# Kernel optimization log

Measured on AMD Instinct MI355X. Metric: run time of the kernel, lower is better.

Reference implementation:

```python
import jax, jax.numpy as jnp
import numpy as np

B, N, D, S = 16, 128, 128, 128   # batch, n_nodes, node/edge feat dim, state_dim
MP_INT = 256
UP_INT = 256
EPS = 1e-3  # keras BatchNormalization default epsilon


def _mlp(x, W1, b1, W2, b2):
    # Dense(relu) -> Dense(relu)
    h = jax.nn.relu(x @ W1 + b1)
    return jax.nn.relu(h @ W2 + b2)


def setup_inputs() -> dict:
    key = jax.random.key(0)
    ks = jax.random.split(key, 16)
    g = lambda k, shape: jax.random.normal(k, shape, dtype=jnp.float32) * 0.05
    nodes = jax.random.normal(ks[0], (B, N, D), dtype=jnp.float32)
    edges = jax.random.normal(ks[1], (B, N * N, D), dtype=jnp.float32)
    mask = (jax.random.uniform(ks[2], (B, N * N, 1)) > 0.5).astype(jnp.float32)
    return {
        "nodes": nodes, "edges": edges, "mask": mask,
        # Adj_Updater_1: concat(node_i, node_j, edge_ij) -> UP_INT -> S
        "W1a": g(ks[3], (3 * D, UP_INT)), "b1a": jnp.zeros((UP_INT,), jnp.float32),
        "W2a": g(ks[4], (UP_INT, S)), "b2a": jnp.zeros((S,), jnp.float32),
        # Message_Passer_1: concat(node_i, node_j, new_edge) -> MP_INT -> S
        "W1m": g(ks[5], (2 * D + S, MP_INT)), "b1m": jnp.zeros((MP_INT,), jnp.float32),
        "W2m": g(ks[6], (MP_INT, S)), "b2m": jnp.zeros((S,), jnp.float32),
        # Update_Func_1: concat(old_state, agg_messages) -> UP_INT -> S
        "W1u": g(ks[7], (D + S, UP_INT)), "b1u": jnp.zeros((UP_INT,), jnp.float32),
        "W2u": g(ks[8], (UP_INT, S)), "b2u": jnp.zeros((S,), jnp.float32),
        # BatchNorm (inference mode: moving stats) for nodes and edges
        "gamma_n": jnp.ones((S,), jnp.float32), "beta_n": jnp.zeros((S,), jnp.float32),
        "mean_n": jnp.zeros((S,), jnp.float32), "var_n": jnp.ones((S,), jnp.float32),
        "gamma_e": jnp.ones((S,), jnp.float32), "beta_e": jnp.zeros((S,), jnp.float32),
        "mean_e": jnp.zeros((S,), jnp.float32), "var_e": jnp.ones((S,), jnp.float32),
    }


def reference(nodes, edges, mask,
              W1a, b1a, W2a, b2a,
              W1m, b1m, W2m, b2m,
              W1u, b1u, W2u, b2u,
              gamma_n, beta_n, mean_n, var_n,
              gamma_e, beta_e, mean_e, var_e):
    b, n, d = nodes.shape
    # tf.tile(nodes,[1,n,1]): row p*n+q -> nodes[q]  (state_i)
    state_i = jnp.broadcast_to(nodes[:, None, :, :], (b, n, n, d)).reshape(b, n * n, d)
    # reshape(tile(nodes,[1,1,n])): row p*n+q -> nodes[p]  (state_j)
    state_j = jnp.broadcast_to(nodes[:, :, None, :], (b, n, n, d)).reshape(b, n * n, d)

    new_edges = _mlp(jnp.concatenate([state_i, state_j, edges], axis=-1), W1a, b1a, W2a, b2a)
    new_edges = new_edges * mask

    messages = _mlp(jnp.concatenate([state_i, state_j, new_edges], axis=-1), W1m, b1m, W2m, b2m)
    masked = (messages * mask).reshape(b, n, n, -1)
    agg_m = masked.sum(axis=2)  # reduce over axis 2 as in Message_Agg

    state_1 = _mlp(jnp.concatenate([nodes, agg_m], axis=-1), W1u, b1u, W2u, b2u)

    bn = lambda x, g_, b_, m_, v_: g_ * (x - m_) * jax.lax.rsqrt(v_ + EPS) + b_
    nodes_out = bn(state_1, gamma_n, beta_n, mean_n, var_n)
    edges_out = bn(new_edges, gamma_e, beta_e, mean_e, var_e)
    return nodes_out, edges_out
```

## Files before the change

### kernel.cpp

```cpp
#include <hip/hip_runtime.h>
#include <hip/hip_bf16.h>
#include <cstdint>
#include <cstddef>


typedef __attribute__((ext_vector_type(8))) __bf16 bf16x8;
typedef __attribute__((ext_vector_type(4))) float f32x4;

#define GLDS(gp, lp)                                                        \
  __builtin_amdgcn_global_load_lds(                                         \
      (const __attribute__((address_space(1))) void*)(gp),                  \
      (__attribute__((address_space(3))) void*)(lp), 16, 0, 0)

__device__ inline bf16x8 load8_cvt(const float* __restrict__ p) {
  const float4 a = *(const float4*)p;
  const float4 b = *(const float4*)(p + 4);
  bf16x8 r;
  r[0] = (__bf16)a.x; r[1] = (__bf16)a.y; r[2] = (__bf16)a.z; r[3] = (__bf16)a.w;
  r[4] = (__bf16)b.x; r[5] = (__bf16)b.y; r[6] = (__bf16)b.z; r[7] = (__bf16)b.w;
  return r;
}

__global__ void __launch_bounds__(256) proj_kernel(
    const float* __restrict__ nodes, const float* __restrict__ W1a,
    const float* __restrict__ b1a, const float* __restrict__ W1m,
    const float* __restrict__ b1m, const float* __restrict__ ge,
    const float* __restrict__ be, const float* __restrict__ me,
    const float* __restrict__ ve, float* __restrict__ outP) {
  __shared__ float x[8][128];
  const int mat = blockIdx.y;
  const int t = threadIdx.x;
  const float* W = (mat < 2 ? W1a : W1m) + ((mat & 1) ? 128 * 256 : 0);
  float* out = outP + (size_t)mat * (2048 * 256);
  const int r0 = blockIdx.x * 8;
  for (int i = t; i < 1024; i += 256)
    x[i >> 7][i & 127] = nodes[r0 * 128 + i];
  __syncthreads();
  float bv = 0.f;
  if (mat == 1) bv = b1a[t];
  if (mat == 3) {
    bv = b1m[t];
    const float* We = W1m + 65536;
    float cc = 0.f;
    for (int k = 0; k < 128; ++k) {
      float sc = ge[k] * rsqrtf(ve[k] + 1e-3f);
      float sh = be[k] - me[k] * sc;
      cc -= (sh / sc) * We[k * 256 + t];
    }
    bv += cc;
  }
  float acc[8];
#pragma unroll
  for (int r = 0; r < 8; ++r) acc[r] = bv;
  for (int k = 0; k < 128; ++k) {
    float w = W[k * 256 + t];
#pragma unroll
    for (int r = 0; r < 8; ++r) acc[r] += x[r][k] * w;
  }
  for (int r = 0; r < 8; ++r) out[(size_t)(r0 + r) * 256 + t] = acc[r];
}

__global__ void __launch_bounds__(256) wswz_kernel(
    const float* __restrict__ W1a, const float* __restrict__ W2a,
    const float* __restrict__ W1m, const float* __restrict__ W2m,
    const float* __restrict__ ge, const float* __restrict__ ve,
    __hip_bfloat16* __restrict__ dstp) {
  __bf16* dst = (__bf16*)dstp;
  const int mat = blockIdx.y;
  const float* src;
  __bf16* d;
  int nsh;
  if (mat == 0)      { src = W1a + 65536; d = dst;         nsh = 8; }
  else if (mat == 1) { src = W2a;         d = dst + 32768; nsh = 7; }
  else if (mat == 2) { src = W1m + 65536; d = dst + 65536; nsh = 8; }
  else               { src = W2m;         d = dst + 98304; nsh = 7; }
  const int nmask = (1 << nsh) - 1;
  const int base = (blockIdx.x * 256 + threadIdx.x) * 4;
#pragma unroll
  for (int i = 0; i < 4; ++i) {
    int s = base + i;
    int k = s >> nsh, n = s & nmask;
    float v = src[s];
    if (mat == 2) v *= sqrtf(ve[k] + 1e-3f) / ge[k];
    int g = k >> 3;
    if (nsh == 8) {
      int gs = (g & 8) | ((g ^ n) & 7);
      d[n * 128 + gs * 8 + (k & 7)] = (__bf16)v;
    } else {
      int gs = (g ^ n) & 7;
      d[((k >> 6) << 13) + (n << 6) + (gs << 3) + (k & 7)] = (__bf16)v;
    }
  }
}

__global__ void __launch_bounds__(256, 2) edge_mlp_kernel(
    const float* __restrict__ edges, const float* __restrict__ mask,
    const float* __restrict__ b2a, const float* __restrict__ ge,
    const float* __restrict__ be, const float* __restrict__ me,
    const float* __restrict__ ve, const float* __restrict__ Pa,
    const float* __restrict__ Qab, const __hip_bfloat16* __restrict__ Wsw,
    float* __restrict__ edges_out) {
  __shared__ __align__(16) char sW1h[16384];
  __shared__ __align__(16) char sW2h[16384];
  __shared__ __align__(16) char sH1q[16384];
  __shared__ float sQ[256];
  __shared__ float sB2[128];
  __shared__ float sMask[128];
  __shared__ float sScE[128];
  __shared__ float sShE[128];

  const int t = threadIdx.x;
  const int lane = t & 63, wv = t >> 6;
  const int cl = lane & 15, qd = lane >> 4;
  const int m0 = wv * 32;

  if (t < 128) {
    sB2[t] = b2a[t];
    float sc = ge[t] * rsqrtf(ve[t] + 1e-3f);
    sScE[t] = sc;
    sShE[t] = be[t] - me[t] * sc;
  }

  const int bb = blockIdx.x >> 5;
  const int p0 = (blockIdx.x & 31) * 4;
  const char* gW1base = (const char*)Wsw;
  const char* gW2base = (const char*)(Wsw + 32768);

  for (int tp = 0; tp < 4; ++tp) {
    const int p = p0 + tp;
    __syncthreads();
    sQ[t] = Qab[((bb << 7) + p) * 256 + t];
    if (t < 128) sMask[t] = mask[(bb << 14) + (p << 7) + t];

    const float* Xb = edges + ((size_t)((bb << 14) + (p << 7)) << 7);
    bf16x8 xf[2][4];
#pragma unroll
    for (int mt = 0; mt < 2; ++mt)
#pragma unroll
      for (int ks = 0; ks < 4; ++ks)
        xf[mt][ks] = load8_cvt(Xb + (m0 + mt * 16 + cl) * 128 + ks * 32 + qd * 8);

    f32x4 ne[2][8];
#pragma unroll
    for (int mt = 0; mt < 2; ++mt)
#pragma unroll
      for (int nt = 0; nt < 8; ++nt) {
        float bv = sB2[nt * 16 + cl];
        ne[mt][nt] = (f32x4){bv, bv, bv, bv};
      }

    for (int h = 0; h < 4; ++h) {
      __syncthreads();
      {
        const char* gW1 = gW1base + h * 16384;
        const char* gW2 = gW2base + h * 16384;
        for (int o = wv * 1024; o < 16384; o += 4096) {
          GLDS(gW1 + o + lane * 16, sW1h + o);
          GLDS(gW2 + o + lane * 16, sW2h + o);
        }
      }
      f32x4 a1[2][4];
#pragma unroll
      for (int mt = 0; mt < 2; ++mt)
#pragma unroll
        for (int nt = 0; nt < 4; ++nt) {
          const int col = h * 64 + nt * 16 + cl;
          const int mrow = m0 + mt * 16 + qd * 4;
          const float qv = sQ[col];
          const float* pa = Pa + (size_t)((bb << 7) + mrow) * 256 + col;
          a1[mt][nt] = (f32x4){pa[0] + qv, pa[256] + qv, pa[512] + qv, pa[768] + qv};
        }
      __syncthreads();
#pragma unroll
      for (int ks = 0; ks < 4; ++ks)
#pragma unroll
        for (int nt = 0; nt < 4; ++nt) {
          const int nl = nt * 16 + cl;
          const int g = ks * 4 + qd;
          const int gs = (g & 8) | ((g ^ nl) & 7);
          bf16x8 bw = *(const bf16x8*)(sW1h + nl * 256 + gs * 16);
          a1[0][nt] = __builtin_amdgcn_mfma_f32_16x16x32_bf16(xf[0][ks], bw, a1[0][nt], 0, 0, 0);
          a1[1][nt] = __builtin_amdgcn_mfma_f32_16x16x32_bf16(xf[1][ks], bw, a1[1][nt], 0, 0, 0);
        }
#pragma unroll
      for (int mt = 0; mt < 2; ++mt)
#pragma unroll
        for (int nt = 0; nt < 4; ++nt) {
          const int kq = nt * 16 + cl;
#pragma unroll
          for (int r = 0; r < 4; ++r) {
            const int m = m0 + mt * 16 + qd * 4 + r;
            float v = a1[mt][nt][r];
            v = v > 0.f ? v : 0.f;
            const int gs = ((kq >> 3) ^ m) & 7;
            *(__bf16*)(sH1q + m * 128 + gs * 16 + (kq & 7) * 2) = (__bf16)v;
          }
        }
      __syncthreads();
      bf16x8 hf[2][2];
#pragma unroll
      for (int mt = 0; mt < 2; ++mt)
#pragma unroll
        for (int ks = 0; ks < 2; ++ks) {
          const int m = m0 + mt * 16 + cl;
          const int g = ks * 4 + qd;
          const int gs = (g ^ m) & 7;
          hf[mt][ks] = *(const bf16x8*)(sH1q + m * 128 + gs * 16);
        }
#pragma unroll
      for (int ks = 0; ks < 2; ++ks)
#pragma unroll
        for (int nt = 0; nt < 8; ++nt) {
          const int n = nt * 16 + cl;
          const int g = ks * 4 + qd;
          const int gs = (g ^ n) & 7;
          bf16x8 bw = *(const bf16x8*)(sW2h + n * 128 + gs * 16);
          ne[0][nt] = __builtin_amdgcn_mfma_f32_16x16x32_bf16(hf[0][ks], bw, ne[0][nt], 0, 0, 0);
          ne[1][nt] = __builtin_amdgcn_mfma_f32_16x16x32_bf16(hf[1][ks], bw, ne[1][nt], 0, 0, 0);
        }
    }
    float* Ob = edges_out + ((size_t)((bb << 14) + (p << 7)) << 7);
#pragma unroll
    for (int mt = 0; mt < 2; ++mt)
#pragma unroll
      for (int nt = 0; nt < 8; ++nt) {
        const int col = nt * 16 + cl;
        const float sc = sScE[col], sh = sShE[col];
#pragma unroll
        for (int r = 0; r < 4; ++r) {
          const int m = m0 + mt * 16 + qd * 4 + r;
          float v = ne[mt][nt][r];
          v = v > 0.f ? v : 0.f;
          Ob[m * 128 + col] = (v * sMask[m]) * sc + sh;
        }
      }
  }
}

__global__ void __launch_bounds__(256, 2) msg_mlp_kernel(
    const float* __restrict__ mask, const float* __restrict__ b2m,
    const float* __restrict__ Pm, const float* __restrict__ Qmb,
    const __hip_bfloat16* __restrict__ Wsw, const float* __restrict__ Yedges,
    float* __restrict__ agg) {
  __shared__ __align__(16) char sW1h[16384];
  __shared__ __align__(16) char sW2h[16384];
  __shared__ __align__(16) char sH1q[16384];
  __shared__ float sQ[256];
  __shared__ float sB2[128];
  __shared__ float sMask[128];
  __shared__ float sAgg[512];

  const int t = threadIdx.x;
  const int lane = t & 63, wv = t >> 6;
  const int cl = lane & 15, qd = lane >> 4;
  const int m0 = wv * 32;

  if (t < 128) sB2[t] = b2m[t];

  const int bb = blockIdx.x >> 5;
  const int p0 = (blockIdx.x & 31) * 4;
  const char* gW1base = (const char*)Wsw;
  const char* gW2base = (const char*)(Wsw + 32768);

  for (int tp = 0; tp < 4; ++tp) {
    const int p = p0 + tp;
    __syncthreads();
    sQ[t] = Qmb[((bb << 7) + p) * 256 + t];
    if (t < 128) sMask[t] = mask[(bb << 14) + (p << 7) + t];

    const float* Xb = Yedges + ((size_t)((bb << 14) + (p << 7)) << 7);
    bf16x8 xf[2][4];
#pragma unroll
    for (int mt = 0; mt < 2; ++mt)
#pragma unroll
      for (int ks = 0; ks < 4; ++ks)
        xf[mt][ks] = load8_cvt(Xb + (m0 + mt * 16 + cl) * 128 + ks * 32 + qd * 8);

    f32x4 ms[2][8];
#pragma unroll
    for (int mt = 0; mt < 2; ++mt)
#pragma unroll
      for (int nt = 0; nt < 8; ++nt) {
        float bv = sB2[nt * 16 + cl];
        ms[mt][nt] = (f32x4){bv, bv, bv, bv};
      }

    for (int h = 0; h < 4; ++h) {
      __syncthreads();
      {
        const char* gW1 = gW1base + h * 16384;
        const char* gW2 = gW2base + h * 16384;
        for (int o = wv * 1024; o < 16384; o += 4096) {
          GLDS(gW1 + o + lane * 16, sW1h + o);
          GLDS(gW2 + o + lane * 16, sW2h + o);
        }
      }
      f32x4 a1[2][4];
#pragma unroll
      for (int mt = 0; mt < 2; ++mt)
#pragma unroll
        for (int nt = 0; nt < 4; ++nt) {
          const int col = h * 64 + nt * 16 + cl;
          const int mrow = m0 + mt * 16 + qd * 4;
          const float qv = sQ[col];
          const float* pa = Pm + (size_t)((bb << 7) + mrow) * 256 + col;
          a1[mt][nt] = (f32x4){pa[0] + qv, pa[256] + qv, pa[512] + qv, pa[768] + qv};
        }
      __syncthreads();
#pragma unroll
      for (int ks = 0; ks < 4; ++ks)
#pragma unroll
        for (int nt = 0; nt < 4; ++nt) {
          const int nl = nt * 16 + cl;
          const int g = ks * 4 + qd;
          const int gs = (g & 8) | ((g ^ nl) & 7);
          bf16x8 bw = *(const bf16x8*)(sW1h + nl * 256 + gs * 16);
          a1[0][nt] = __builtin_amdgcn_mfma_f32_16x16x32_bf16(xf[0][ks], bw, a1[0][nt], 0, 0, 0);
          a1[1][nt] = __builtin_amdgcn_mfma_f32_16x16x32_bf16(xf[1][ks], bw, a1[1][nt], 0, 0, 0);
        }
#pragma unroll
      for (int mt = 0; mt < 2; ++mt)
#pragma unroll
        for (int nt = 0; nt < 4; ++nt) {
          const int kq = nt * 16 + cl;
#pragma unroll
          for (int r = 0; r < 4; ++r) {
            const int m = m0 + mt * 16 + qd * 4 + r;
            float v = a1[mt][nt][r];
            v = v > 0.f ? v : 0.f;
            const int gs = ((kq >> 3) ^ m) & 7;
            *(__bf16*)(sH1q + m * 128 + gs * 16 + (kq & 7) * 2) = (__bf16)v;
          }
        }
      __syncthreads();
      bf16x8 hf[2][2];
#pragma unroll
      for (int mt = 0; mt < 2; ++mt)
#pragma unroll
        for (int ks = 0; ks < 2; ++ks) {
          const int m = m0 + mt * 16 + cl;
          const int g = ks * 4 + qd;
          const int gs = (g ^ m) & 7;
          hf[mt][ks] = *(const bf16x8*)(sH1q + m * 128 + gs * 16);
        }
#pragma unroll
      for (int ks = 0; ks < 2; ++ks)
#pragma unroll
        for (int nt = 0; nt < 8; ++nt) {
          const int n = nt * 16 + cl;
          const int g = ks * 4 + qd;
          const int gs = (g ^ n) & 7;
          bf16x8 bw = *(const bf16x8*)(sW2h + n * 128 + gs * 16);
          ms[0][nt] = __builtin_amdgcn_mfma_f32_16x16x32_bf16(hf[0][ks], bw, ms[0][nt], 0, 0, 0);
          ms[1][nt] = __builtin_amdgcn_mfma_f32_16x16x32_bf16(hf[1][ks], bw, ms[1][nt], 0, 0, 0);
        }
    }
#pragma unroll
    for (int nt = 0; nt < 8; ++nt) {
      float s = 0.f;
#pragma unroll
      for (int mt = 0; mt < 2; ++mt)
#pragma unroll
        for (int r = 0; r < 4; ++r) {
          const int m = m0 + mt * 16 + qd * 4 + r;
          float v = ms[mt][nt][r];
          v = v > 0.f ? v : 0.f;
          s += v * sMask[m];
        }
      s += __shfl_xor(s, 16);
      s += __shfl_xor(s, 32);
      if (lane < 16) sAgg[wv * 128 + nt * 16 + lane] = s;
    }
    __syncthreads();
    if (t < 128)
      agg[((bb << 7) + p) * 128 + t] =
          sAgg[t] + sAgg[128 + t] + sAgg[256 + t] + sAgg[384 + t];
  }
}

__global__ void __launch_bounds__(256) update_kernel(
    const float* __restrict__ nodes, const float* __restrict__ agg,
    const float* __restrict__ W1u, const float* __restrict__ b1u,
    const float* __restrict__ W2u, const float* __restrict__ b2u,
    const float* __restrict__ gn, const float* __restrict__ btn,
    const float* __restrict__ mn, const float* __restrict__ vn,
    float* __restrict__ out) {
  __shared__ float x[8][256];
  __shared__ float hh[8][256];
  const int t = threadIdx.x;
  const int r0 = blockIdx.x * 8;
  for (int i = t; i < 2048; i += 256) {
    int r = i >> 8, c = i & 255;
    x[r][c] = (c < 128) ? nodes[(r0 + r) * 128 + c] : agg[(r0 + r) * 128 + (c - 128)];
  }
  __syncthreads();
  float acc[8];
  {
    float bv = b1u[t];
#pragma unroll
    for (int r = 0; r < 8; ++r) acc[r] = bv;
  }
  for (int k = 0; k < 256; ++k) {
    float w = W1u[k * 256 + t];
#pragma unroll
    for (int r = 0; r < 8; ++r) acc[r] += x[r][k] * w;
  }
#pragma unroll
  for (int r = 0; r < 8; ++r) hh[r][t] = acc[r] > 0.f ? acc[r] : 0.f;
  __syncthreads();
  const int j = t & 127, half = t >> 7;
  float a2[4];
  {
    float bv = b2u[j];
#pragma unroll
    for (int r = 0; r < 4; ++r) a2[r] = bv;
  }
  for (int k = 0; k < 256; ++k) {
    float w = W2u[k * 128 + j];
#pragma unroll
    for (int r = 0; r < 4; ++r) a2[r] += hh[half * 4 + r][k] * w;
  }
  float sc = gn[j] * rsqrtf(vn[j] + 1e-3f);
  float sh = btn[j] - mn[j] * sc;
#pragma unroll
  for (int r = 0; r < 4; ++r) {
    float v = a2[r] > 0.f ? a2[r] : 0.f;
    out[(r0 + half * 4 + r) * 128 + j] = v * sc + sh;
  }
}

extern "C" void kernel_launch(void* const* d_in, const int* in_sizes, int n_in,
                              void* d_out, int out_size, void* d_ws,
                              size_t ws_size, hipStream_t stream) {
  (void)in_sizes; (void)n_in; (void)out_size; (void)ws_size;
  const float* nodes = (const float*)d_in[0];
  const float* edges = (const float*)d_in[1];
  const float* mask = (const float*)d_in[2];
  const float* W1a = (const float*)d_in[3];
  const float* b1a = (const float*)d_in[4];
  const float* W2a = (const float*)d_in[5];
  const float* b2a = (const float*)d_in[6];
  const float* W1m = (const float*)d_in[7];
  const float* b1m = (const float*)d_in[8];
  const float* W2m = (const float*)d_in[9];
  const float* b2m = (const float*)d_in[10];
  const float* W1u = (const float*)d_in[11];
  const float* b1u = (const float*)d_in[12];
  const float* W2u = (const float*)d_in[13];
  const float* b2u = (const float*)d_in[14];
  const float* gn = (const float*)d_in[15];
  const float* btn = (const float*)d_in[16];
  const float* mn = (const float*)d_in[17];
  const float* vn = (const float*)d_in[18];
  const float* ge = (const float*)d_in[19];
  const float* be = (const float*)d_in[20];
  const float* me = (const float*)d_in[21];
  const float* ve = (const float*)d_in[22];

  float* out_nodes = (float*)d_out;
  float* out_edges = (float*)d_out + 262144;

  char* ws = (char*)d_ws;
  float* Pa = (float*)(ws);
  float* Qab = (float*)(ws + ((size_t)1 << 21));
  float* Pm = (float*)(ws + ((size_t)2 << 21));
  float* Qmb = (float*)(ws + ((size_t)3 << 21));
  float* agg = (float*)(ws + ((size_t)4 << 21));
  __hip_bfloat16* Wsw = (__hip_bfloat16*)(ws + ((size_t)4 << 21) + ((size_t)1 << 20));

  proj_kernel<<<dim3(256, 4), 256, 0, stream>>>(nodes, W1a, b1a, W1m, b1m, ge,
                                                be, me, ve, Pa);
  wswz_kernel<<<dim3(32, 4), 256, 0, stream>>>(W1a, W2a, W1m, W2m, ge, ve, Wsw);
  edge_mlp_kernel<<<512, 256, 0, stream>>>(edges, mask, b2a, ge, be, me, ve, Pa,
                                           Qab, Wsw, out_edges);
  msg_mlp_kernel<<<512, 256, 0, stream>>>(mask, b2m, Pm, Qmb, Wsw + 65536,
                                          out_edges, agg);
  update_kernel<<<256, 256, 0, stream>>>(nodes, agg, W1u, b1u, W2u, b2u, gn, btn,
                                         mn, vn, out_nodes);
}
```

Before: 454.1 us.

## Fuse edge and message MLP kernels, keeping new edges in LDS

Merges the edge-update MLP and the message MLP into one kernel. The masked pre-BatchNorm edge tile is written to LDS as bf16 and used directly as the message MLP input, so the fp32 edges_out is no longer reloaded from global memory. The BatchNorm-fold adjustments to the message weights and bias are removed because the raw masked edges are now used. Each block handles one (batch,row) instead of four, giving 2048 blocks, and launch bounds rise to 3 blocks per CU. This costs a larger LDS arena and more register pressure per block, and weights are now loaded twice per row-pair.

```diff
diff --git a/kernel.cpp b/kernel.cpp
--- a/kernel.cpp
+++ b/kernel.cpp
@@ -24,9 +24,7 @@
 __global__ void __launch_bounds__(256) proj_kernel(
     const float* __restrict__ nodes, const float* __restrict__ W1a,
     const float* __restrict__ b1a, const float* __restrict__ W1m,
-    const float* __restrict__ b1m, const float* __restrict__ ge,
-    const float* __restrict__ be, const float* __restrict__ me,
-    const float* __restrict__ ve, float* __restrict__ outP) {
+    const float* __restrict__ b1m, float* __restrict__ outP) {
   __shared__ float x[8][128];
   const int mat = blockIdx.y;
   const int t = threadIdx.x;
@@ -38,17 +36,7 @@
   __syncthreads();
   float bv = 0.f;
   if (mat == 1) bv = b1a[t];
-  if (mat == 3) {
-    bv = b1m[t];
-    const float* We = W1m + 65536;
-    float cc = 0.f;
-    for (int k = 0; k < 128; ++k) {
-      float sc = ge[k] * rsqrtf(ve[k] + 1e-3f);
-      float sh = be[k] - me[k] * sc;
-      cc -= (sh / sc) * We[k * 256 + t];
-    }
-    bv += cc;
-  }
+  if (mat == 3) bv = b1m[t];
   float acc[8];
 #pragma unroll
   for (int r = 0; r < 8; ++r) acc[r] = bv;
@@ -63,7 +51,6 @@
 __global__ void __launch_bounds__(256) wswz_kernel(
     const float* __restrict__ W1a, const float* __restrict__ W2a,
     const float* __restrict__ W1m, const float* __restrict__ W2m,
-    const float* __restrict__ ge, const float* __restrict__ ve,
     __hip_bfloat16* __restrict__ dstp) {
   __bf16* dst = (__bf16*)dstp;
   const int mat = blockIdx.y;
@@ -81,7 +68,6 @@
     int s = base + i;
     int k = s >> nsh, n = s & nmask;
     float v = src[s];
-    if (mat == 2) v *= sqrtf(ve[k] + 1e-3f) / ge[k];
     int g = k >> 3;
     if (nsh == 8) {
       int gs = (g & 8) | ((g ^ n) & 7);
@@ -93,18 +79,23 @@
   }
 }
 
-__global__ void __launch_bounds__(256, 2) edge_mlp_kernel(
+__global__ void __launch_bounds__(256, 3) fused_mlp_kernel(
     const float* __restrict__ edges, const float* __restrict__ mask,
-    const float* __restrict__ b2a, const float* __restrict__ ge,
-    const float* __restrict__ be, const float* __restrict__ me,
-    const float* __restrict__ ve, const float* __restrict__ Pa,
-    const float* __restrict__ Qab, const __hip_bfloat16* __restrict__ Wsw,
-    float* __restrict__ edges_out) {
-  __shared__ __align__(16) char sW1h[16384];
-  __shared__ __align__(16) char sW2h[16384];
-  __shared__ __align__(16) char sH1q[16384];
+    const float* __restrict__ b2a, const float* __restrict__ b2m,
+    const float* __restrict__ ge, const float* __restrict__ be,
+    const float* __restrict__ me, const float* __restrict__ ve,
+    const float* __restrict__ Pa, const float* __restrict__ Qab,
+    const float* __restrict__ Pm, const float* __restrict__ Qmb,
+    const __hip_bfloat16* __restrict__ Wsw, float* __restrict__ edges_out,
+    float* __restrict__ agg) {
+  __shared__ __align__(16) char sArena[49152];
+  char* const sW1h = sArena;
+  char* const sW2h = sArena + 16384;
+  char* const sH1q = sArena + 32768;
+  float* const sAgg = (float*)(sArena + 32768);
   __shared__ float sQ[256];
-  __shared__ float sB2[128];
+  __shared__ float sB2a[128];
+  __shared__ float sB2m[128];
   __shared__ float sMask[128];
   __shared__ float sScE[128];
   __shared__ float sShE[128];
@@ -114,111 +105,114 @@
   const int cl = lane & 15, qd = lane >> 4;
   const int m0 = wv * 32;
 
+  const int bb = blockIdx.x >> 7;
+  const int p = blockIdx.x & 127;
+
   if (t < 128) {
-    sB2[t] = b2a[t];
+    sB2a[t] = b2a[t];
+    sB2m[t] = b2m[t];
     float sc = ge[t] * rsqrtf(ve[t] + 1e-3f);
     sScE[t] = sc;
     sShE[t] = be[t] - me[t] * sc;
-  }
-
-  const int bb = blockIdx.x >> 5;
-  const int p0 = (blockIdx.x & 31) * 4;
-  const char* gW1base = (const char*)Wsw;
-  const char* gW2base = (const char*)(Wsw + 32768);
-
-  for (int tp = 0; tp < 4; ++tp) {
-    const int p = p0 + tp;
-    __syncthreads();
-    sQ[t] = Qab[((bb << 7) + p) * 256 + t];
-    if (t < 128) sMask[t] = mask[(bb << 14) + (p << 7) + t];
-
-    const float* Xb = edges + ((size_t)((bb << 14) + (p << 7)) << 7);
-    bf16x8 xf[2][4];
-#pragma unroll
-    for (int mt = 0; mt < 2; ++mt)
-#pragma unroll
-      for (int ks = 0; ks < 4; ++ks)
-        xf[mt][ks] = load8_cvt(Xb + (m0 + mt * 16 + cl) * 128 + ks * 32 + qd * 8);
-
-    f32x4 ne[2][8];
-#pragma unroll
-    for (int mt = 0; mt < 2; ++mt)
+    sMask[t] = mask[(bb << 14) + (p << 7) + t];
+  }
+  sQ[t] = Qab[((bb << 7) + p) * 256 + t];
+  __syncthreads();
+
+  const float* Xb = edges + ((size_t)((bb << 14) + (p << 7)) << 7);
+  bf16x8 xf[2][4];
+#pragma unroll
+  for (int mt = 0; mt < 2; ++mt)
+#pragma unroll
+    for (int ks = 0; ks < 4; ++ks)
+      xf[mt][ks] = load8_cvt(Xb + (m0 + mt * 16 + cl) * 128 + ks * 32 + qd * 8);
+
+  f32x4 ne[2][8];
+#pragma unroll
+  for (int mt = 0; mt < 2; ++mt)
+#pragma unroll
+    for (int nt = 0; nt < 8; ++nt) {
+      float bv = sB2a[nt * 16 + cl];
+      ne[mt][nt] = (f32x4){bv, bv, bv, bv};
+    }
+
+  const char* gW1e = (const char*)Wsw;
+  const char* gW2e = (const char*)(Wsw + 32768);
+
+  for (int h = 0; h < 4; ++h) {
+    __syncthreads();
+    {
+      const char* gW1 = gW1e + h * 16384;
+      const char* gW2 = gW2e + h * 16384;
+      for (int o = wv * 1024; o < 16384; o += 4096) {
+        GLDS(gW1 + o + lane * 16, sW1h + o);
+        GLDS(gW2 + o + lane * 16, sW2h + o);
+      }
+    }
+    f32x4 a1[2][4];
+#pragma unroll
+    for (int mt = 0; mt < 2; ++mt)
+#pragma unroll
+      for (int nt = 0; nt < 4; ++nt) {
+        const int col = h * 64 + nt * 16 + cl;
+        const int mrow = m0 + mt * 16 + qd * 4;
+        const float qv = sQ[col];
+        const float* pa = Pa + (size_t)((bb << 7) + mrow) * 256 + col;
+        a1[mt][nt] = (f32x4){pa[0] + qv, pa[256] + qv, pa[512] + qv, pa[768] + qv};
+      }
+    __syncthreads();
+#pragma unroll
+    for (int ks = 0; ks < 4; ++ks)
+#pragma unroll
+      for (int nt = 0; nt < 4; ++nt) {
+        const int nl = nt * 16 + cl;
+        const int g = ks * 4 + qd;
+        const int gs = (g & 8) | ((g ^ nl) & 7);
+        bf16x8 bw = *(const bf16x8*)(sW1h + nl * 256 + gs * 16);
+        a1[0][nt] = __builtin_amdgcn_mfma_f32_16x16x32_bf16(xf[0][ks], bw, a1[0][nt], 0, 0, 0);
+        a1[1][nt] = __builtin_amdgcn_mfma_f32_16x16x32_bf16(xf[1][ks], bw, a1[1][nt], 0, 0, 0);
+      }
+#pragma unroll
+    for (int mt = 0; mt < 2; ++mt)
+#pragma unroll
+      for (int nt = 0; nt < 4; ++nt) {
+        const int kq = nt * 16 + cl;
+#pragma unroll
+        for (int r = 0; r < 4; ++r) {
+          const int m = m0 + mt * 16 + qd * 4 + r;
+          float v = a1[mt][nt][r];
+          v = v > 0.f ? v : 0.f;
+          const int gs = ((kq >> 3) ^ m) & 7;
+          *(__bf16*)(sH1q + m * 128 + gs * 16 + (kq & 7) * 2) = (__bf16)v;
+        }
+      }
+    __syncthreads();
+    bf16x8 hf[2][2];
+#pragma unroll
+    for (int mt = 0; mt < 2; ++mt)
+#pragma unroll
+      for (int ks = 0; ks < 2; ++ks) {
+        const int m = m0 + mt * 16 + cl;
+        const int g = ks * 4 + qd;
+        const int gs = (g ^ m) & 7;
+        hf[mt][ks] = *(const bf16x8*)(sH1q + m * 128 + gs * 16);
+      }
+#pragma unroll
+    for (int ks = 0; ks < 2; ++ks)
 #pragma unroll
       for (int nt = 0; nt < 8; ++nt) {
-        float bv = sB2[nt * 16 + cl];
-        ne[mt][nt] = (f32x4){bv, bv, bv, bv};
-      }
-
-    for (int h = 0; h < 4; ++h) {
-      __syncthreads();
-      {
-        const char* gW1 = gW1base + h * 16384;
-        const char* gW2 = gW2base + h * 16384;
-        for (int o = wv * 1024; o < 16384; o += 4096) {
-          GLDS(gW1 + o + lane * 16, sW1h + o);
-          GLDS(gW2 + o + lane * 16, sW2h + o);
-        }
-      }
-      f32x4 a1[2][4];
-#pragma unroll
-      for (int mt = 0; mt < 2; ++mt)
-#pragma unroll
-        for (int nt = 0; nt < 4; ++nt) {
-          const int col = h * 64 + nt * 16 + cl;
-          const int mrow = m0 + mt * 16 + qd * 4;
-          const float qv = sQ[col];
-          const float* pa = Pa + (size_t)((bb << 7) + mrow) * 256 + col;
-          a1[mt][nt] = (f32x4){pa[0] + qv, pa[256] + qv, pa[512] + qv, pa[768] + qv};
-        }
-      __syncthreads();
-#pragma unroll
-      for (int ks = 0; ks < 4; ++ks)
-#pragma unroll
-        for (int nt = 0; nt < 4; ++nt) {
-          const int nl = nt * 16 + cl;
-          const int g = ks * 4 + qd;
-          const int gs = (g & 8) | ((g ^ nl) & 7);
-          bf16x8 bw = *(const bf16x8*)(sW1h + nl * 256 + gs * 16);
-          a1[0][nt] = __builtin_amdgcn_mfma_f32_16x16x32_bf16(xf[0][ks], bw, a1[0][nt], 0, 0, 0);
-          a1[1][nt] = __builtin_amdgcn_mfma_f32_16x16x32_bf16(xf[1][ks], bw, a1[1][nt], 0, 0, 0);
-        }
-#pragma unroll
-      for (int mt = 0; mt < 2; ++mt)
-#pragma unroll
-        for (int nt = 0; nt < 4; ++nt) {
-          const int kq = nt * 16 + cl;
-#pragma unroll
-          for (int r = 0; r < 4; ++r) {
-            const int m = m0 + mt * 16 + qd * 4 + r;
-            float v = a1[mt][nt][r];
-            v = v > 0.f ? v : 0.f;
-            const int gs = ((kq >> 3) ^ m) & 7;
-            *(__bf16*)(sH1q + m * 128 + gs * 16 + (kq & 7) * 2) = (__bf16)v;
-          }
-        }
-      __syncthreads();
-      bf16x8 hf[2][2];
-#pragma unroll
-      for (int mt = 0; mt < 2; ++mt)
-#pragma unroll
-        for (int ks = 0; ks < 2; ++ks) {
-          const int m = m0 + mt * 16 + cl;
-          const int g = ks * 4 + qd;
-          const int gs = (g ^ m) & 7;
-          hf[mt][ks] = *(const bf16x8*)(sH1q + m * 128 + gs * 16);
-        }
-#pragma unroll
-      for (int ks = 0; ks < 2; ++ks)
-#pragma unroll
-        for (int nt = 0; nt < 8; ++nt) {
-          const int n = nt * 16 + cl;
-          const int g = ks * 4 + qd;
-          const int gs = (g ^ n) & 7;
-          bf16x8 bw = *(const bf16x8*)(sW2h + n * 128 + gs * 16);
-          ne[0][nt] = __builtin_amdgcn_mfma_f32_16x16x32_bf16(hf[0][ks], bw, ne[0][nt], 0, 0, 0);
-          ne[1][nt] = __builtin_amdgcn_mfma_f32_16x16x32_bf16(hf[1][ks], bw, ne[1][nt], 0, 0, 0);
-        }
-    }
+        const int n = nt * 16 + cl;
+        const int g = ks * 4 + qd;
+        const int gs = (g ^ n) & 7;
+        bf16x8 bw = *(const bf16x8*)(sW2h + n * 128 + gs * 16);
+        ne[0][nt] = __builtin_amdgcn_mfma_f32_16x16x32_bf16(hf[0][ks], bw, ne[0][nt], 0, 0, 0);
+        ne[1][nt] = __builtin_amdgcn_mfma_f32_16x16x32_bf16(hf[1][ks], bw, ne[1][nt], 0, 0, 0);
+      }
+  }
+
+  __syncthreads();
+  sQ[t] = Qmb[((bb << 7) + p) * 256 + t];
+  {
     float* Ob = edges_out + ((size_t)((bb << 14) + (p << 7)) << 7);
 #pragma unroll
     for (int mt = 0; mt < 2; ++mt)
@@ -226,156 +220,143 @@
       for (int nt = 0; nt < 8; ++nt) {
         const int col = nt * 16 + cl;
         const float sc = sScE[col], sh = sShE[col];
+        char* const buf = (nt & 4) ? sW2h : sW1h;
+        const int kq = col & 63;
 #pragma unroll
         for (int r = 0; r < 4; ++r) {
           const int m = m0 + mt * 16 + qd * 4 + r;
           float v = ne[mt][nt][r];
           v = v > 0.f ? v : 0.f;
-          Ob[m * 128 + col] = (v * sMask[m]) * sc + sh;
+          const float e = v * sMask[m];
+          Ob[m * 128 + col] = e * sc + sh;
+          const int gs = ((kq >> 3) ^ m) & 7;
+          *(__bf16*)(buf + m * 128 + gs * 16 + (kq & 7) * 2) = (__bf16)e;
         }
       }
   }
-}
-
-__global__ void __launch_bounds__(256, 2) msg_mlp_kernel(
-    const float* __restrict__ mask, const float* __restrict__ b2m,
-    const float* __restrict__ Pm, const float* __restrict__ Qmb,
-    const __hip_bfloat16* __restrict__ Wsw, const float* __restrict__ Yedges,
-    float* __restrict__ agg) {
-  __shared__ __align__(16) char sW1h[16384];
-  __shared__ __align__(16) char sW2h[16384];
-  __shared__ __align__(16) char sH1q[16384];
-  __shared__ float sQ[256];
-  __shared__ float sB2[128];
-  __shared__ float sMask[128];
-  __shared__ float sAgg[512];
-
-  const int t = threadIdx.x;
-  const int lane = t & 63, wv = t >> 6;
-  const int cl = lane & 15, qd = lane >> 4;
-  const int m0 = wv * 32;
-
-  if (t < 128) sB2[t] = b2m[t];
-
-  const int bb = blockIdx.x >> 5;
-  const int p0 = (blockIdx.x & 31) * 4;
-  const char* gW1base = (const char*)Wsw;
-  const char* gW2base = (const char*)(Wsw + 32768);
-
-  for (int tp = 0; tp < 4; ++tp) {
-    const int p = p0 + tp;
-    __syncthreads();
-    sQ[t] = Qmb[((bb << 7) + p) * 256 + t];
-    if (t < 128) sMask[t] = mask[(bb << 14) + (p << 7) + t];
-
-    const float* Xb = Yedges + ((size_t)((bb << 14) + (p << 7)) << 7);
-    bf16x8 xf[2][4];
-#pragma unroll
-    for (int mt = 0; mt < 2; ++mt)
-#pragma unroll
-      for (int ks = 0; ks < 4; ++ks)
-        xf[mt][ks] = load8_cvt(Xb + (m0 + mt * 16 + cl) * 128 + ks * 32 + qd * 8);
-
-    f32x4 ms[2][8];
-#pragma unroll
-    for (int mt = 0; mt < 2; ++mt)
-#pragma unroll
-      for (int nt = 0; nt < 8; ++nt) {
-        float bv = sB2[nt * 16 + cl];
-        ms[mt][nt] = (f32x4){bv, bv, bv, bv};
-      }
-
-    for (int h = 0; h < 4; ++h) {
-      __syncthreads();
-      {
-        const char* gW1 = gW1base + h * 16384;
-        const char* gW2 = gW2base + h * 16384;
-        for (int o = wv * 1024; o < 16384; o += 4096) {
-          GLDS(gW1 + o + lane * 16, sW1h + o);
-          GLDS(gW2 + o + lane * 16, sW2h + o);
-        }
-      }
-      f32x4 a1[2][4];
-#pragma unroll
-      for (int mt = 0; mt < 2; ++mt)
-#pragma unroll
-        for (int nt = 0; nt < 4; ++nt) {
-          const int col = h * 64 + nt * 16 + cl;
-          const int mrow = m0 + mt * 16 + qd * 4;
-          const float qv = sQ[col];
-          const float* pa = Pm + (size_t)((bb << 7) + mrow) * 256 + col;
-          a1[mt][nt] = (f32x4){pa[0] + qv, pa[256] + qv, pa[512] + qv, pa[768] + qv};
-        }
-      __syncthreads();
-#pragma unroll
-      for (int ks = 0; ks < 4; ++ks)
-#pragma unroll
-        for (int nt = 0; nt < 4; ++nt) {
-          const int nl = nt * 16 + cl;
-          const int g = ks * 4 + qd;
-          const int gs = (g & 8) | ((g ^ nl) & 7);
-          bf16x8 bw = *(const bf16x8*)(sW1h + nl * 256 + gs * 16);
-          a1[0][nt] = __builtin_amdgcn_mfma_f32_16x16x32_bf16(xf[0][ks], bw, a1[0][nt], 0, 0, 0);
-          a1[1][nt] = __builtin_amdgcn_mfma_f32_16x16x32_bf16(xf[1][ks], bw, a1[1][nt], 0, 0, 0);
-        }
-#pragma unroll
-      for (int mt = 0; mt < 2; ++mt)
-#pragma unroll
-        for (int nt = 0; nt < 4; ++nt) {
-          const int kq = nt * 16 + cl;
-#pragma unroll
-          for (int r = 0; r < 4; ++r) {
-            const int m = m0 + mt * 16 + qd * 4 + r;
-            float v = a1[mt][nt][r];
-            v = v > 0.f ? v : 0.f;
-            const int gs = ((kq >> 3) ^ m) & 7;
-            *(__bf16*)(sH1q + m * 128 + gs * 16 + (kq & 7) * 2) = (__bf16)v;
-          }
-        }
-      __syncthreads();
-      bf16x8 hf[2][2];
-#pragma unroll
-      for (int mt = 0; mt < 2; ++mt)
-#pragma unroll
-        for (int ks = 0; ks < 2; ++ks) {
-          const int m = m0 + mt * 16 + cl;
-          const int g = ks * 4 + qd;
-          const int gs = (g ^ m) & 7;
-          hf[mt][ks] = *(const bf16x8*)(sH1q + m * 128 + gs * 16);
-        }
-#pragma unroll
-      for (int ks = 0; ks < 2; ++ks)
-#pragma unroll
-        for (int nt = 0; nt < 8; ++nt) {
-          const int n = nt * 16 + cl;
-          const int g = ks * 4 + qd;
-          const int gs = (g ^ n) & 7;
-          bf16x8 bw = *(const bf16x8*)(sW2h + n * 128 + gs * 16);
-          ms[0][nt] = __builtin_amdgcn_mfma_f32_16x16x32_bf16(hf[0][ks], bw, ms[0][nt], 0, 0, 0);
-          ms[1][nt] = __builtin_amdgcn_mfma_f32_16x16x32_bf16(hf[1][ks], bw, ms[1][nt], 0, 0, 0);
-        }
-    }
+  __syncthreads();
+
+  bf16x8 xf2[2][4];
+#pragma unroll
+  for (int mt = 0; mt < 2; ++mt)
+#pragma unroll
+    for (int ks = 0; ks < 4; ++ks) {
+      const int m = m0 + mt * 16 + cl;
+      const int g = (ks & 1) * 4 + qd;
+      const int gs = (g ^ m) & 7;
+      const char* buf = (ks & 2) ? sW2h : sW1h;
+      xf2[mt][ks] = *(const bf16x8*)(buf + m * 128 + gs * 16);
+    }
+
+  f32x4 ms[2][8];
+#pragma unroll
+  for (int mt = 0; mt < 2; ++mt)
 #pragma unroll
     for (int nt = 0; nt < 8; ++nt) {
-      float s = 0.f;
-#pragma unroll
-      for (int mt = 0; mt < 2; ++mt)
+      float bv = sB2m[nt * 16 + cl];
+      ms[mt][nt] = (f32x4){bv, bv, bv, bv};
+    }
+
+  const char* gW1m = (const char*)(Wsw + 65536);
+  const char* gW2m = (const char*)(Wsw + 98304);
+
+  for (int h = 0; h < 4; ++h) {
+    __syncthreads();
+    {
+      const char* gW1 = gW1m + h * 16384;
+      const char* gW2 = gW2m + h * 16384;
+      for (int o = wv * 1024; o < 16384; o += 4096) {
+        GLDS(gW1 + o + lane * 16, sW1h + o);
+        GLDS(gW2 + o + lane * 16, sW2h + o);
+      }
+    }
+    f32x4 a1[2][4];
+#pragma unroll
+    for (int mt = 0; mt < 2; ++mt)
+#pragma unroll
+      for (int nt = 0; nt < 4; ++nt) {
+        const int col = h * 64 + nt * 16 + cl;
+        const int mrow = m0 + mt * 16 + qd * 4;
+        const float qv = sQ[col];
+        const float* pa = Pm + (size_t)((bb << 7) + mrow) * 256 + col;
+        a1[mt][nt] = (f32x4){pa[0] + qv, pa[256] + qv, pa[512] + qv, pa[768] + qv};
+      }
+    __syncthreads();
+#pragma unroll
+    for (int ks = 0; ks < 4; ++ks)
+#pragma unroll
+      for (int nt = 0; nt < 4; ++nt) {
+        const int nl = nt * 16 + cl;
+        const int g = ks * 4 + qd;
+        const int gs = (g & 8) | ((g ^ nl) & 7);
+        bf16x8 bw = *(const bf16x8*)(sW1h + nl * 256 + gs * 16);
+        a1[0][nt] = __builtin_amdgcn_mfma_f32_16x16x32_bf16(xf2[0][ks], bw, a1[0][nt], 0, 0, 0);
+        a1[1][nt] = __builtin_amdgcn_mfma_f32_16x16x32_bf16(xf2[1][ks], bw, a1[1][nt], 0, 0, 0);
+      }
+#pragma unroll
+    for (int mt = 0; mt < 2; ++mt)
+#pragma unroll
+      for (int nt = 0; nt < 4; ++nt) {
+        const int kq = nt * 16 + cl;
 #pragma unroll
         for (int r = 0; r < 4; ++r) {
           const int m = m0 + mt * 16 + qd * 4 + r;
-          float v = ms[mt][nt][r];
+          float v = a1[mt][nt][r];
           v = v > 0.f ? v : 0.f;
-          s += v * sMask[m];
+          const int gs = ((kq >> 3) ^ m) & 7;
+          *(__bf16*)(sH1q + m * 128 + gs * 16 + (kq & 7) * 2) = (__bf16)v;
         }
-      s += __shfl_xor(s, 16);
-      s += __shfl_xor(s, 32);
-      if (lane < 16) sAgg[wv * 128 + nt * 16 + lane] = s;
-    }
-    __syncthreads();
-    if (t < 128)
-      agg[((bb << 7) + p) * 128 + t] =
-          sAgg[t] + sAgg[128 + t] + sAgg[256 + t] + sAgg[384 + t];
-  }
+      }
+    __syncthreads();
+    bf16x8 hf[2][2];
+#pragma unroll
+    for (int mt = 0; mt < 2; ++mt)
+#pragma unroll
+      for (int ks = 0; ks < 2; ++ks) {
+        const int m = m0 + mt * 16 + cl;
+        const int g = ks * 4 + qd;
+        const int gs = (g ^ m) & 7;
+        hf[mt][ks] = *(const bf16x8*)(sH1q + m * 128 + gs * 16);
+      }
+#pragma unroll
+    for (int ks = 0; ks < 2; ++ks)
+#pragma unroll
+      for (int nt = 0; nt < 8; ++nt) {
+        const int n = nt * 16 + cl;
+        const int g = ks * 4 + qd;
+        const int gs = (g ^ n) & 7;
+        bf16x8 bw = *(const bf16x8*)(sW2h + n * 128 + gs * 16);
+        ms[0][nt] = __builtin_amdgcn_mfma_f32_16x16x32_bf16(hf[0][ks], bw, ms[0][nt], 0, 0, 0);
+        ms[1][nt] = __builtin_amdgcn_mfma_f32_16x16x32_bf16(hf[1][ks], bw, ms[1][nt], 0, 0, 0);
+      }
+  }
+
+  float ss[8];
+#pragma unroll
+  for (int nt = 0; nt < 8; ++nt) {
+    float s = 0.f;
+#pragma unroll
+    for (int mt = 0; mt < 2; ++mt)
+#pragma unroll
+      for (int r = 0; r < 4; ++r) {
+        const int m = m0 + mt * 16 + qd * 4 + r;
+        float v = ms[mt][nt][r];
+        v = v > 0.f ? v : 0.f;
+        s += v * sMask[m];
+      }
+    s += __shfl_xor(s, 16);
+    s += __shfl_xor(s, 32);
+    ss[nt] = s;
+  }
+  __syncthreads();
+  if (lane < 16) {
+#pragma unroll
+    for (int nt = 0; nt < 8; ++nt) sAgg[wv * 128 + nt * 16 + lane] = ss[nt];
+  }
+  __syncthreads();
+  if (t < 128)
+    agg[((bb << 7) + p) * 128 + t] =
+        sAgg[t] + sAgg[128 + t] + sAgg[256 + t] + sAgg[384 + t];
 }
 
 __global__ void __launch_bounds__(256) update_kernel(
@@ -468,13 +449,11 @@
   float* agg = (float*)(ws + ((size_t)4 << 21));
   __hip_bfloat16* Wsw = (__hip_bfloat16*)(ws + ((size_t)4 << 21) + ((size_t)1 << 20));
 
-  proj_kernel<<<dim3(256, 4), 256, 0, stream>>>(nodes, W1a, b1a, W1m, b1m, ge,
-                                                be, me, ve, Pa);
-  wswz_kernel<<<dim3(32, 4), 256, 0, stream>>>(W1a, W2a, W1m, W2m, ge, ve, Wsw);
-  edge_mlp_kernel<<<512, 256, 0, stream>>>(edges, mask, b2a, ge, be, me, ve, Pa,
-                                           Qab, Wsw, out_edges);
-  msg_mlp_kernel<<<512, 256, 0, stream>>>(mask, b2m, Pm, Qmb, Wsw + 65536,
-                                          out_edges, agg);
+  proj_kernel<<<dim3(256, 4), 256, 0, stream>>>(nodes, W1a, b1a, W1m, b1m, Pa);
+  wswz_kernel<<<dim3(32, 4), 256, 0, stream>>>(W1a, W2a, W1m, W2m, Wsw);
+  fused_mlp_kernel<<<2048, 256, 0, stream>>>(edges, mask, b2a, b2m, ge, be, me,
+                                             ve, Pa, Qab, Pm, Qmb, Wsw,
+                                             out_edges, agg);
   update_kernel<<<256, 256, 0, stream>>>(nodes, agg, W1u, b1u, W2u, b2u, gn, btn,
                                          mn, vn, out_nodes);
 }
```

Result: slower. 524.6 us (+15.5%).
